# Performance work log

Measured on AMD Instinct MI355X. Metric: run time of the kernel, lower is better.

Reference implementation:

```python
import jax, jax.numpy as jnp
import numpy as np

B, T = 128, 50
VOCAB, EMB_D, GRU_H = 10000, 200, 100
HEADS, AHID, THID = 8, 96, 96

def _conv(x, w, b, pad):
    y = jax.lax.conv_general_dilated(x, w, (1, 1), pad,
        dimension_numbers=('NCHW', 'OIHW', 'NCHW'))
    return y + b[None, :, None, None]

def _bn(x, g, b, m, v):
    s = jax.lax.rsqrt(v + 1e-5)
    return (x - m[None, :, None, None]) * (g * s)[None, :, None, None] + b[None, :, None, None]

def _maxpool(x):
    return jax.lax.reduce_window(x, -jnp.inf, jax.lax.max, (1, 1, 2, 2), (1, 1, 2, 2), 'VALID')

def _resize(x):
    # F.interpolate(mode='bilinear', align_corners=False) == half-pixel bilinear, no antialias
    return jax.image.resize(x, (x.shape[0], x.shape[1], 25, 156), 'bilinear', antialias=False)

def _audio_attn(x, wq, bq, wk, bk, wv, bv):
    # x: [B,96,H,W]; wq: [heads,96,96] == stacked per-head 1x1 convs
    Q = jnp.einsum('bchw,noc->bnohw', x, wq) + bq[None, :, :, None, None]
    K = jnp.einsum('bchw,noc->bnohw', x, wk) + bk[None, :, :, None, None]
    V = jnp.einsum('bchw,noc->bnohw', x, wv) + bv[None, :, :, None, None]
    # torch F.softmax with no dim on a 4D tensor defaults to dim=1 (channels) -> axis=2 here
    return jax.nn.softmax(Q * K, axis=2) * V  # [B,heads,96,H,W]

def _text_attn(o, wq, bq, wk, bk, wv, bv):
    # o: [N,100]; wq: [heads,96,100] == stacked per-head Linear layers
    Q = jnp.einsum('nd,hod->nho', o, wq) + bq[None]
    K = jnp.einsum('nd,hod->nho', o, wk) + bk[None]
    V = jnp.einsum('nd,hod->nho', o, wv) + bv[None]
    a = jax.nn.softmax(Q * K, axis=2) * V  # 2D softmax default dim=1 -> over feature axis
    return a.reshape(o.shape[0], -1)  # head-concat order == torch cat along dim=1

def _gru(xs, w_ih, w_hh, b_ih, b_hh):
    # xs: [T,B,200]; torch gate order r, z, n; b_hn applied inside r-gating
    def step(h, x):
        gi = x @ w_ih.T + b_ih
        gh = h @ w_hh.T + b_hh
        ir, iz, inew = jnp.split(gi, 3, axis=1)
        hr, hz, hnew = jnp.split(gh, 3, axis=1)
        r = jax.nn.sigmoid(ir + hr)
        z = jax.nn.sigmoid(iz + hz)
        n = jnp.tanh(inew + r * hnew)
        h2 = (1.0 - z) * n + z * h
        return h2, h2
    h0 = jnp.zeros((xs.shape[1], GRU_H), xs.dtype)
    hT, outs = jax.lax.scan(step, h0, xs)
    return outs, hT

def _forward(tokens, lengths, mfcc_t, mfcc_f, mfcc_c, w1a, b1a, g1a, be1a, m1a, v1a, w1b, b1b, g1b, be1b, m1b, v1b, w2, b2, g2, be2, m2, v2, w3, b3, g3, be3, m3, v3, w4, b4, g4, be4, m4, v4, wq_a1, bq_a1, wk_a1, bk_a1, wv_a1, bv_a1, wq_a2, bq_a2, wk_a2, bk_a2, wv_a2, bv_a2, emb, w_ih, w_hh, b_ih, b_hh, wq_t1, bq_t1, wk_t1, bk_t1, wv_t1, bv_t1, wq_t2, bq_t2, wk_t2, bk_t2, wv_t2, bv_t2, w_fa, b_fa, w_ft, b_ft, w_e, b_e):
    # --- audio CNN stem (eval-mode batchnorm; dropout off) ---
    xa = jax.nn.relu(_bn(_conv(mfcc_t, w1a, b1a, 'VALID'), g1a, be1a, m1a, v1a))
    xb = jax.nn.relu(_bn(_conv(mfcc_f, w1b, b1b, 'VALID'), g1b, be1b, m1b, v1b))
    # NOTE: original source reuses conv1b/bn1b for the third input (faithful to that)
    xc = jax.nn.relu(_bn(_conv(mfcc_c, w1b, b1b, 'VALID'), g1b, be1b, m1b, v1b))
    x = jnp.concatenate([_resize(xa), _resize(xb), _resize(xc)], axis=1)  # [B,24,25,156]
    x = _maxpool(jax.nn.relu(_bn(_conv(x, w2, b2, [(1, 1), (1, 1)]), g2, be2, m2, v2)))  # [B,32,12,78]
    x = _maxpool(jax.nn.relu(_bn(_conv(x, w3, b3, [(1, 1), (1, 1)]), g3, be3, m3, v3)))  # [B,64,6,39]
    x = jax.nn.relu(_bn(_conv(x, w4, b4, [(1, 1), (1, 1)]), g4, be4, m4, v4))            # [B,96,6,39]
    # --- two stacked per-head audio attentions, then per-head spatial GAP ---
    a1 = _audio_attn(x, wq_a1, bq_a1, wk_a1, bk_a1, wv_a1, bv_a1).mean(axis=(-2, -1))  # [B,8,96]
    a2 = _audio_attn(x, wq_a2, bq_a2, wk_a2, bk_a2, wv_a2, bv_a2).mean(axis=(-2, -1))
    # forward() slices heads along the height concat and GAPs -> per head [stage1 96, stage2 96]
    self_attn_audio = jnp.concatenate([a1, a2], axis=2).reshape(x.shape[0], -1)  # [B,1536]
    # --- text branch: embedding + GRU (all lengths == T -> pack/pad is identity) ---
    ex = jnp.swapaxes(emb[tokens], 0, 1)  # [T,B,200]
    outs, h = _gru(ex, w_ih, w_hh, b_ih, b_hh)  # h: [B,100]
    output = jnp.swapaxes(outs, 0, 1).reshape(-1, GRU_H)  # [B*T,100]
    t1 = _text_attn(output, wq_t1, bq_t1, wk_t1, bk_t1, wv_t1, bv_t1)
    t2 = _text_attn(output, wq_t2, bq_t2, wk_t2, bk_t2, wv_t2, bv_t2)
    self_attn_text = jnp.concatenate([t1, t2], axis=1).reshape(x.shape[0], T, -1).sum(axis=1)  # [B,1536]
    # --- cross-modal gated fusion ---
    x_gap = x.mean(axis=(-2, -1))  # [B,96]
    a_text = jax.nn.softmax(x_gap @ w_fa.T + b_fa, axis=1)   # [B,100]
    attn_text_based_audio = a_text * h                        # [B,100]
    a_audio = jax.nn.softmax(h @ w_ft.T + b_ft, axis=1)      # [B,96]
    attn_audio_based_text = a_audio * x_gap                   # [B,96]
    feat = jnp.concatenate([self_attn_audio, self_attn_text,
                            attn_audio_based_text, attn_text_based_audio], axis=1)  # [B,3268]
    return feat @ w_e.T + b_e  # [B,4] emotion logits

def setup_inputs() -> dict:
    key = jax.random.key(0)
    ks = iter(jax.random.split(key, 100))
    nrm = lambda s, sc=0.05: jax.random.normal(next(ks), s, jnp.float32) * sc
    uni = lambda s: jax.random.uniform(next(ks), s, jnp.float32) * 0.5 + 0.5
    d = {}
    d['mfcc_t'] = jax.random.normal(next(ks), (B, 1, 200, 40), jnp.float32)
    d['mfcc_f'] = jax.random.normal(next(ks), (B, 1, 200, 40), jnp.float32)
    d['mfcc_c'] = jax.random.normal(next(ks), (B, 1, 200, 40), jnp.float32)
    d['tokens'] = jax.random.randint(next(ks), (B, T), 0, VOCAB)
    d['lengths'] = jnp.full((B,), T, jnp.int32)
    def bnp(pre, c):
        d['g' + pre] = 1.0 + nrm((c,)); d['be' + pre] = nrm((c,))
        d['m' + pre] = nrm((c,)); d['v' + pre] = uni((c,))
    d['w1a'] = nrm((8, 1, 5, 2), 0.2); d['b1a'] = nrm((8,)); bnp('1a', 8)
    d['w1b'] = nrm((8, 1, 2, 6), 0.2); d['b1b'] = nrm((8,)); bnp('1b', 8)
    d['w2'] = nrm((32, 24, 3, 3), 0.1); d['b2'] = nrm((32,)); bnp('2', 32)
    d['w3'] = nrm((64, 32, 3, 3), 0.1); d['b3'] = nrm((64,)); bnp('3', 64)
    d['w4'] = nrm((96, 64, 3, 3), 0.08); d['b4'] = nrm((96,)); bnp('4', 96)
    for s in ('1', '2'):
        for p in ('q', 'k', 'v'):
            d['w%s_a%s' % (p, s)] = nrm((HEADS, 96, 96), 0.1)
            d['b%s_a%s' % (p, s)] = nrm((HEADS, 96))
    d['emb'] = nrm((VOCAB, EMB_D), 0.1)
    d['w_ih'] = nrm((3 * GRU_H, EMB_D), 0.1); d['w_hh'] = nrm((3 * GRU_H, GRU_H), 0.1)
    d['b_ih'] = nrm((3 * GRU_H,)); d['b_hh'] = nrm((3 * GRU_H,))
    for s in ('1', '2'):
        for p in ('q', 'k', 'v'):
            d['w%s_t%s' % (p, s)] = nrm((HEADS, THID, GRU_H), 0.1)
            d['b%s_t%s' % (p, s)] = nrm((HEADS, THID))
    d['w_fa'] = nrm((100, 96), 0.1); d['b_fa'] = nrm((100,))
    d['w_ft'] = nrm((96, 100), 0.1); d['b_ft'] = nrm((96,))
    d['w_e'] = nrm((4, 2 * HEADS * AHID + 2 * HEADS * THID + 96 + 100), 0.05); d['b_e'] = nrm((4,))
    return d

def reference(mfcc_t, mfcc_f, mfcc_c, tokens, lengths, w1a, b1a, g1a, be1a, m1a, v1a, w1b, b1b, g1b, be1b, m1b, v1b, w2, b2, g2, be2, m2, v2, w3, b3, g3, be3, m3, v3, w4, b4, g4, be4, m4, v4, wq_a1, bq_a1, wk_a1, bk_a1, wv_a1, bv_a1, wq_a2, bq_a2, wk_a2, bk_a2, wv_a2, bv_a2, emb, w_ih, w_hh, b_ih, b_hh, wq_t1, bq_t1, wk_t1, bk_t1, wv_t1, bv_t1, wq_t2, bq_t2, wk_t2, bk_t2, wv_t2, bv_t2, w_fa, b_fa, w_ft, b_ft, w_e, b_e):
    return _forward(tokens, lengths, mfcc_t, mfcc_f, mfcc_c, w1a, b1a, g1a, be1a, m1a, v1a, w1b, b1b, g1b, be1b, m1b, v1b, w2, b2, g2, be2, m2, v2, w3, b3, g3, be3, m3, v3, w4, b4, g4, be4, m4, v4, wq_a1, bq_a1, wk_a1, bk_a1, wv_a1, bv_a1, wq_a2, bq_a2, wk_a2, bk_a2, wv_a2, bv_a2, emb, w_ih, w_hh, b_ih, b_hh, wq_t1, bq_t1, wk_t1, bk_t1, wv_t1, bv_t1, wq_t2, bq_t2, wk_t2, bk_t2, wv_t2, bv_t2, w_fa, b_fa, w_ft, b_ft, w_e, b_e)
```

## Files before the change

### kernel.cpp

```cpp
#include <hip/hip_runtime.h>
#include <math.h>

static constexpr int kB = 128;
static constexpr int kT = 50;

struct TDesc { const float* src; float* dst; int O; int C; int total; };
struct TPack { TDesc d[15]; };
__global__ void k_transpose_pack(TPack p) {
    TDesc t = p.d[blockIdx.y];
    int idx = blockIdx.x * 256 + threadIdx.x;
    if (idx >= t.total) return;
    int o = idx % t.O; int r = idx / t.O; int c = r % t.C; int n = r / t.C;
    t.dst[idx] = t.src[((size_t)n * t.O + o) * t.C + c];
}

__global__ void k_stem(const float* __restrict__ mt, const float* __restrict__ mf,
                       const float* __restrict__ mc,
                       const float* __restrict__ w1a, const float* __restrict__ b1a,
                       const float* __restrict__ g1a, const float* __restrict__ be1a,
                       const float* __restrict__ m1a, const float* __restrict__ v1a,
                       const float* __restrict__ w1b, const float* __restrict__ b1b,
                       const float* __restrict__ g1b, const float* __restrict__ be1b,
                       const float* __restrict__ m1b, const float* __restrict__ v1b,
                       float* __restrict__ out, int total) {
    int idx = blockIdx.x * blockDim.x + threadIdx.x;
    if (idx >= total) return;
    int ox = idx % 156; int t = idx / 156;
    int oy = t % 25; t /= 25;
    int ch = t % 24; int b = t / 24;
    int grp = ch >> 3, c = ch & 7;
    const float* src; int Hc, Wc;
    const float *wb, *cb, *g, *be, *m, *v;
    if (grp == 0) { src = mt; Hc = 196; Wc = 39; wb = w1a + c * 10;
                    cb = b1a; g = g1a; be = be1a; m = m1a; v = v1a; }
    else          { src = (grp == 1 ? mf : mc); Hc = 199; Wc = 35; wb = w1b + c * 12;
                    cb = b1b; g = g1b; be = be1b; m = m1b; v = v1b; }
    float s = g[c] * rsqrtf(v[c] + 1e-5f);
    float bias = (cb[c] - m[c]) * s + be[c];
    float sy = (oy + 0.5f) * ((float)Hc / 25.f) - 0.5f;
    float sx = (ox + 0.5f) * ((float)Wc / 156.f) - 0.5f;
    float fy0 = floorf(sy), fx0 = floorf(sx);
    float fy = sy - fy0, fx = sx - fx0;
    int y0 = (int)fy0, x0 = (int)fx0;
    int y0c = min(max(y0, 0), Hc - 1), y1c = min(max(y0 + 1, 0), Hc - 1);
    int x0c = min(max(x0, 0), Wc - 1), x1c = min(max(x0 + 1, 0), Wc - 1);
    bool xs = (x1c == x0c), ys = (y1c == y0c);
    const float* p = src + (size_t)b * 8000;
    float t00, t01, t10, t11;
    if (grp == 0) {
        float W[6][3];
        #pragma unroll
        for (int r = 0; r < 6; ++r) {
            int rr = min(y0c + r, 199);
            #pragma unroll
            for (int cc = 0; cc < 3; ++cc)
                W[r][cc] = p[rr * 40 + min(x0c + cc, 39)];
        }
        float a00 = 0.f, a01 = 0.f, a10 = 0.f, a11 = 0.f;
        #pragma unroll
        for (int ky = 0; ky < 5; ++ky)
            #pragma unroll
            for (int kx = 0; kx < 2; ++kx) {
                float wv = wb[ky * 2 + kx];
                a00 += W[ky][kx] * wv;     a01 += W[ky][kx + 1] * wv;
                a10 += W[ky + 1][kx] * wv; a11 += W[ky + 1][kx + 1] * wv;
            }
        t00 = a00;
        t01 = xs ? a00 : a01;
        t10 = ys ? a00 : a10;
        t11 = xs ? (ys ? a00 : a10) : (ys ? a01 : a11);
    } else {
        float W[3][7];
        #pragma unroll
        for (int r = 0; r < 3; ++r) {
            int rr = min(y0c + r, 199);
            #pragma unroll
            for (int cc = 0; cc < 7; ++cc)
                W[r][cc] = p[rr * 40 + min(x0c + cc, 39)];
        }
        float a00 = 0.f, a01 = 0.f, a10 = 0.f, a11 = 0.f;
        #pragma unroll
        for (int ky = 0; ky < 2; ++ky)
            #pragma unroll
            for (int kx = 0; kx < 6; ++kx) {
                float wv = wb[ky * 6 + kx];
                a00 += W[ky][kx] * wv;     a01 += W[ky][kx + 1] * wv;
                a10 += W[ky + 1][kx] * wv; a11 += W[ky + 1][kx + 1] * wv;
            }
        t00 = a00;
        t01 = xs ? a00 : a01;
        t10 = ys ? a00 : a10;
        t11 = xs ? (ys ? a00 : a10) : (ys ? a01 : a11);
    }
    float r00 = fmaxf(t00 * s + bias, 0.f), r01 = fmaxf(t01 * s + bias, 0.f);
    float r10 = fmaxf(t10 * s + bias, 0.f), r11 = fmaxf(t11 * s + bias, 0.f);
    out[idx] = r00 * (1.f - fy) * (1.f - fx) + r01 * (1.f - fy) * fx
             + r10 * fy * (1.f - fx) + r11 * fy * fx;
}

template<int CIN, int CI_T, int H, int W, int ROWS, int NPX>
__global__ void __launch_bounds__(256) k_conv3x3_tiled(
    const float* __restrict__ in, const float* __restrict__ wT,
    const float* __restrict__ cb, const float* __restrict__ g,
    const float* __restrict__ be, const float* __restrict__ m,
    const float* __restrict__ v, float* __restrict__ out, int COUT) {
    constexpr int WP = W + 2;
    constexpr int RP = ROWS + 2;
    constexpr int STAGE = CI_T * RP * WP;
    __shared__ float sx[STAGE];
    __shared__ float sw[CI_T * 9 * 8];
    const int b = blockIdx.x, rt = blockIdx.y, oc0 = blockIdx.z * 8;
    const int row0 = rt * ROWS;
    const int tid = threadIdx.x;

    int off[NPX]; bool val[NPX];
    #pragma unroll
    for (int j = 0; j < NPX; ++j) {
        int px = tid + j * 256;
        int oy = px / W, ox = px - oy * W;
        bool ok = (px < ROWS * W) && (row0 + oy < H);
        val[j] = ok;
        off[j] = ok ? (oy * WP + ox) : 0;
    }

    float acc[NPX][8];
    #pragma unroll
    for (int j = 0; j < NPX; ++j)
        #pragma unroll
        for (int o = 0; o < 8; ++o) acc[j][o] = 0.f;

    for (int c0 = 0; c0 < CIN; c0 += CI_T) {
        __syncthreads();
        for (int e = tid; e < STAGE; e += 256) {
            int ci = e / (RP * WP);
            int rem = e - ci * RP * WP;
            int r = rem / WP;
            int xx = rem - r * WP;
            int iy = row0 - 1 + r;
            int ix = xx - 1;
            float vv = 0.f;
            if (iy >= 0 && iy < H && ix >= 0 && ix < W)
                vv = in[((size_t)(b * CIN + c0 + ci) * H + iy) * W + ix];
            sx[e] = vv;
        }
        for (int e = tid; e < CI_T * 9 * 8; e += 256) {
            int rk = e >> 3;
            int o = e & 7;
            sw[e] = wT[((size_t)c0 * 9 + rk) * COUT + oc0 + o];
        }
        __syncthreads();
        #pragma unroll 1
        for (int cl = 0; cl < CI_T; ++cl) {
            const float* sxc = sx + cl * RP * WP;
            #pragma unroll
            for (int k = 0; k < 9; ++k) {
                const int ky = k / 3, kx = k % 3;
                const float4 wa = *(const float4*)(sw + (cl * 9 + k) * 8);
                const float4 wb = *(const float4*)(sw + (cl * 9 + k) * 8 + 4);
                #pragma unroll
                for (int j = 0; j < NPX; ++j) {
                    float xv = sxc[off[j] + ky * WP + kx];
                    acc[j][0] += xv * wa.x; acc[j][1] += xv * wa.y;
                    acc[j][2] += xv * wa.z; acc[j][3] += xv * wa.w;
                    acc[j][4] += xv * wb.x; acc[j][5] += xv * wb.y;
                    acc[j][6] += xv * wb.z; acc[j][7] += xv * wb.w;
                }
            }
        }
    }
    float sc[8], bi[8];
    #pragma unroll
    for (int o = 0; o < 8; ++o) {
        float s = g[oc0 + o] * rsqrtf(v[oc0 + o] + 1e-5f);
        sc[o] = s; bi[o] = (cb[oc0 + o] - m[oc0 + o]) * s + be[oc0 + o];
    }
    #pragma unroll
    for (int j = 0; j < NPX; ++j) if (val[j]) {
        int px = tid + j * 256;
        int oy = row0 + px / W, ox = px % W;
        #pragma unroll
        for (int o = 0; o < 8; ++o)
            out[((size_t)(b * COUT + oc0 + o) * H + oy) * W + ox] =
                fmaxf(acc[j][o] * sc[o] + bi[o], 0.f);
    }
}

__global__ void k_maxpool(const float* __restrict__ in, float* __restrict__ out,
                          int C, int Hin, int Win, int Hout, int Wout, int total) {
    int idx = blockIdx.x * blockDim.x + threadIdx.x;
    if (idx >= total) return;
    int ox = idx % Wout; int t = idx / Wout;
    int oy = t % Hout; t /= Hout;
    int c = t % C; int b = t / C;
    const float* p = in + ((size_t)(b * C + c) * Hin + 2 * oy) * Win + 2 * ox;
    float m0 = fmaxf(p[0], p[1]);
    float m1 = fmaxf(p[Win], p[Win + 1]);
    out[idx] = fmaxf(m0, m1);
}

__global__ void __launch_bounds__(128) k_audio_attn(
    const float* __restrict__ x,
    const float* __restrict__ wq1, const float* __restrict__ bq1,
    const float* __restrict__ wk1, const float* __restrict__ bk1,
    const float* __restrict__ wv1, const float* __restrict__ bv1,
    const float* __restrict__ wq2, const float* __restrict__ bq2,
    const float* __restrict__ wk2, const float* __restrict__ bk2,
    const float* __restrict__ wv2, const float* __restrict__ bv2,
    float* __restrict__ afeat, float* __restrict__ xgap) {
    int b = blockIdx.x, n = blockIdx.y, stage = blockIdx.z;
    const float* wq = stage ? wq2 : wq1; const float* bq = stage ? bq2 : bq1;
    const float* wk = stage ? wk2 : wk1; const float* bk = stage ? bk2 : bk1;
    const float* wv = stage ? wv2 : wv1; const float* bv = stage ? bv2 : bv1;
    __shared__ float xt[96 * 28];
    __shared__ float sb[96 * 27];
    __shared__ float pmax[4][26], psum[4][26];
    __shared__ float mx[26], sm[26];
    int tid = threadIdx.x;
    bool act = tid < 96;
    int o = act ? tid : 0;
    float bqv = act ? bq[n * 96 + tid] : 0.f;
    float bkv = act ? bk[n * 96 + tid] : 0.f;
    float bvv = act ? bv[n * 96 + tid] : 0.f;
    const float* wqb = wq + n * 9216 + o;
    const float* wkb = wk + n * 9216 + o;
    const float* wvb = wv + n * 9216 + o;
    const bool do_gap = (n == 0 && stage == 0);
    float accO = 0.f, xsum = 0.f;
    const float* xb = x + (size_t)b * 96 * 234;
    for (int tile = 0; tile < 9; ++tile) {
        int p0 = tile * 26;
        __syncthreads();
        for (int e = tid; e < 2496; e += 128) {
            int c = e / 26, pp = e - c * 26;
            xt[c * 28 + pp] = xb[c * 234 + p0 + pp];
        }
        __syncthreads();
        if (do_gap && act) {
            const float* xr = xt + o * 28;
            #pragma unroll
            for (int p = 0; p < 26; ++p) xsum += xr[p];
        }
        float aq[26], ak[26], av[26];
        #pragma unroll
        for (int p = 0; p < 26; ++p) { aq[p] = bqv; ak[p] = bkv; av[p] = bvv; }
        for (int c = 0; c < 96; ++c) {
            float wqv = wqb[c * 96], wkv = wkb[c * 96], wvv2 = wvb[c * 96];
            const float* xr = xt + c * 28;
            #pragma unroll
            for (int q4 = 0; q4 < 6; ++q4) {
                float4 x4 = *(const float4*)(xr + q4 * 4);
                int p = q4 * 4;
                aq[p]   += wqv * x4.x; ak[p]   += wkv * x4.x; av[p]   += wvv2 * x4.x;
                aq[p+1] += wqv * x4.y; ak[p+1] += wkv * x4.y; av[p+1] += wvv2 * x4.y;
                aq[p+2] += wqv * x4.z; ak[p+2] += wkv * x4.z; av[p+2] += wvv2 * x4.z;
                aq[p+3] += wqv * x4.w; ak[p+3] += wkv * x4.w; av[p+3] += wvv2 * x4.w;
            }
            float2 x2 = *(const float2*)(xr + 24);
            aq[24] += wqv * x2.x; ak[24] += wkv * x2.x; av[24] += wvv2 * x2.x;
            aq[25] += wqv * x2.y; ak[25] += wkv * x2.y; av[25] += wvv2 * x2.y;
        }
        if (act) {
            #pragma unroll
            for (int p = 0; p < 26; ++p)
                sb[o * 27 + p] = aq[p] * ak[p];
        }
        __syncthreads();
        if (tid < 104) {
            int p = tid % 26, ch = tid / 26;
            int o0 = ch * 24;
            float m_ = -1e30f;
            for (int q = 0; q < 24; ++q) m_ = fmaxf(m_, sb[(o0 + q) * 27 + p]);
            pmax[ch][p] = m_;
        }
        __syncthreads();
        if (tid < 26)
            mx[tid] = fmaxf(fmaxf(pmax[0][tid], pmax[1][tid]),
                            fmaxf(pmax[2][tid], pmax[3][tid]));
        __syncthreads();
        if (tid < 104) {
            int p = tid % 26, ch = tid / 26;
            int o0 = ch * 24;
            float mv = mx[p];
            float s_ = 0.f;
            for (int q = 0; q < 24; ++q) s_ += __expf(sb[(o0 + q) * 27 + p] - mv);
            psum[ch][p] = s_;
        }
        __syncthreads();
        if (tid < 26)
            sm[tid] = psum[0][tid] + psum[1][tid] + psum[2][tid] + psum[3][tid];
        __syncthreads();
        if (act) {
            #pragma unroll
            for (int p = 0; p < 26; ++p)
                accO += __expf(sb[o * 27 + p] - mx[p]) / sm[p] * av[p];
        }
    }
    if (act) afeat[b * 1536 + n * 192 + stage * 96 + tid] = accO * (1.f / 234.f);
    if (do_gap && act) xgap[b * 96 + tid] = xsum * (1.f / 234.f);
}

__global__ void __launch_bounds__(320) k_gi(const int* __restrict__ tokens,
        const float* __restrict__ emb, const float* __restrict__ w_ih,
        const float* __restrict__ b_ih, float* __restrict__ GI) {
    int r0 = blockIdx.x * 8;
    int tid = threadIdx.x;
    __shared__ float er[8][200];
    for (int e = tid; e < 1600; e += 320) {
        int r = e / 200, c = e - r * 200;
        er[r][c] = emb[(size_t)tokens[r0 + r] * 200 + c];
    }
    __syncthreads();
    if (tid < 300) {
        float acc[8];
        float bv = b_ih[tid];
        #pragma unroll
        for (int r = 0; r < 8; ++r) acc[r] = bv;
        for (int k4 = 0; k4 < 50; ++k4) {
            float4 w4 = *(const float4*)(w_ih + (size_t)tid * 200 + k4 * 4);
            #pragma unroll
            for (int r = 0; r < 8; ++r) {
                float4 x4 = *(const float4*)&er[r][k4 * 4];
                acc[r] += w4.x * x4.x + w4.y * x4.y + w4.z * x4.z + w4.w * x4.w;
            }
        }
        #pragma unroll
        for (int r = 0; r < 8; ++r)
            GI[(size_t)(r0 + r) * 300 + tid] = acc[r];
    }
}

__global__ void __launch_bounds__(320) k_gru_all(const float* __restrict__ GI,
        const float* __restrict__ w_hh, const float* __restrict__ b_hh,
        float* __restrict__ outs) {
    int b = blockIdx.x, tid = threadIdx.x;
    __shared__ float hs[100];
    __shared__ float gH[300];
    float4 wreg[25];
    float bias = 0.f;
    if (tid < 300) {
        bias = b_hh[tid];
        #pragma unroll
        for (int k4 = 0; k4 < 25; ++k4)
            wreg[k4] = *(const float4*)(w_hh + (size_t)tid * 100 + k4 * 4);
    }
    if (tid < 100) hs[tid] = 0.f;
    __syncthreads();
    for (int t = 0; t < kT; ++t) {
        if (tid < 300) {
            float gh = bias;
            #pragma unroll
            for (int k4 = 0; k4 < 25; ++k4) {
                float4 h4 = *(const float4*)&hs[k4 * 4];
                gh += wreg[k4].x * h4.x + wreg[k4].y * h4.y
                    + wreg[k4].z * h4.z + wreg[k4].w * h4.w;
            }
            gH[tid] = gh;
        }
        __syncthreads();
        if (tid < 100) {
            const float* gi = GI + ((size_t)b * kT + t) * 300;
            float r = 1.f / (1.f + expf(-(gi[tid] + gH[tid])));
            float z = 1.f / (1.f + expf(-(gi[100 + tid] + gH[100 + tid])));
            float nn = tanhf(gi[200 + tid] + r * gH[200 + tid]);
            float h2 = (1.f - z) * nn + z * hs[tid];
            hs[tid] = h2;
            outs[((size_t)b * kT + t) * 100 + tid] = h2;
        }
        __syncthreads();
    }
}

__global__ void __launch_bounds__(128) k_text_attn(const float* __restrict__ outs,
    const float* __restrict__ wq1, const float* __restrict__ bq1,
    const float* __restrict__ wk1, const float* __restrict__ bk1,
    const float* __restrict__ wv1, const float* __restrict__ bv1,
    const float* __restrict__ wq2, const float* __restrict__ bq2,
    const float* __restrict__ wk2, const float* __restrict__ bk2,
    const float* __restrict__ wv2, const float* __restrict__ bv2,
    float* __restrict__ tfeat) {
    int b = blockIdx.x, stage = blockIdx.y, n = blockIdx.z;
    const float* wq = stage ? wq2 : wq1; const float* bq = stage ? bq2 : bq1;
    const float* wk = stage ? wk2 : wk1; const float* bk = stage ? bk2 : bk1;
    const float* wv = stage ? wv2 : wv1; const float* bv = stage ? bv2 : bv1;
    int tid = threadIdx.x;
    bool act = tid < 96;
    int oo = act ? tid : 0;
    const float* wqc = wq + n * 9600 + oo;
    const float* wkc = wk + n * 9600 + oo;
    const float* wvc = wv + n * 9600 + oo;
    float bqv = act ? bq[n * 96 + tid] : 0.f;
    float bkv = act ? bk[n * 96 + tid] : 0.f;
    float bvv = act ? bv[n * 96 + tid] : 0.f;
    __shared__ float rows[10][100];
    __shared__ float wredM[2][10], wredS[2][10];
    float acc = 0.f;
    int wave = tid >> 6, lane = tid & 63;
    for (int tile = 0; tile < 5; ++tile) {
        int t0 = tile * 10;
        __syncthreads();
        for (int e = tid; e < 1000; e += 128) {
            int tt = e / 100, c = e - tt * 100;
            rows[tt][c] = outs[((size_t)b * kT + t0 + tt) * 100 + c];
        }
        __syncthreads();
        float q[10], k[10], v[10];
        #pragma unroll
        for (int tt = 0; tt < 10; ++tt) { q[tt] = bqv; k[tt] = bkv; v[tt] = bvv; }
        for (int c4 = 0; c4 < 25; ++c4) {
            int cb = c4 * 4 * 96;
            float q0 = wqc[cb], q1 = wqc[cb + 96], q2 = wqc[cb + 192], q3 = wqc[cb + 288];
            float k0 = wkc[cb], k1 = wkc[cb + 96], k2 = wkc[cb + 192], k3 = wkc[cb + 288];
            float v0 = wvc[cb], v1 = wvc[cb + 96], v2 = wvc[cb + 192], v3 = wvc[cb + 288];
            #pragma unroll
            for (int tt = 0; tt < 10; ++tt) {
                float4 x4 = *(const float4*)&rows[tt][c4 * 4];
                q[tt] += q0 * x4.x + q1 * x4.y + q2 * x4.z + q3 * x4.w;
                k[tt] += k0 * x4.x + k1 * x4.y + k2 * x4.z + k3 * x4.w;
                v[tt] += v0 * x4.x + v1 * x4.y + v2 * x4.z + v3 * x4.w;
            }
        }
        float s[10], e_[10];
        #pragma unroll
        for (int tt = 0; tt < 10; ++tt) s[tt] = act ? q[tt] * k[tt] : -1e30f;
        #pragma unroll
        for (int tt = 0; tt < 10; ++tt) {
            float m = s[tt];
            #pragma unroll
            for (int off = 1; off < 64; off <<= 1) m = fmaxf(m, __shfl_xor(m, off));
            if (lane == 0) wredM[wave][tt] = m;
        }
        __syncthreads();
        #pragma unroll
        for (int tt = 0; tt < 10; ++tt) {
            float mx = fmaxf(wredM[0][tt], wredM[1][tt]);
            e_[tt] = expf(s[tt] - mx);
        }
        #pragma unroll
        for (int tt = 0; tt < 10; ++tt) {
            float sm = e_[tt];
            #pragma unroll
            for (int off = 1; off < 64; off <<= 1) sm += __shfl_xor(sm, off);
            if (lane == 0) wredS[wave][tt] = sm;
        }
        __syncthreads();
        #pragma unroll
        for (int tt = 0; tt < 10; ++tt) {
            float sm = wredS[0][tt] + wredS[1][tt];
            acc += e_[tt] / sm * v[tt];
        }
    }
    if (act) tfeat[b * 1536 + stage * 768 + n * 96 + tid] = acc;
}

__global__ void __launch_bounds__(128) k_final(const float* __restrict__ xgap,
    const float* __restrict__ outs, const float* __restrict__ afeat,
    const float* __restrict__ tfeat,
    const float* __restrict__ w_fa, const float* __restrict__ b_fa,
    const float* __restrict__ w_ft, const float* __restrict__ b_ft,
    const float* __restrict__ w_e, const float* __restrict__ b_e,
    float* __restrict__ out) {
    int b = blockIdx.x; int tid = threadIdx.x;
    __shared__ float xg[96], hv[100], st[100], sa[96], aat[96], atba[100];
    __shared__ float redm[2], reds[2];
    if (tid < 96) xg[tid] = xgap[b * 96 + tid];
    if (tid < 100) hv[tid] = outs[(size_t)(b * kT + kT - 1) * 100 + tid];
    __syncthreads();
    if (tid < 100) {
        float acc = b_fa[tid];
        const float* wr = w_fa + tid * 96;
        for (int c = 0; c < 96; ++c) acc += wr[c] * xg[c];
        st[tid] = acc;
    }
    if (tid < 96) {
        float acc = b_ft[tid];
        const float* wr = w_ft + tid * 100;
        for (int c = 0; c < 100; ++c) acc += wr[c] * hv[c];
        sa[tid] = acc;
    }
    __syncthreads();
    if (tid == 0) {
        float mxv = -1e30f; for (int i = 0; i < 100; ++i) mxv = fmaxf(mxv, st[i]);
        float s = 0.f; for (int i = 0; i < 100; ++i) s += expf(st[i] - mxv);
        redm[0] = mxv; reds[0] = s;
    }
    if (tid == 1) {
        float mxv = -1e30f; for (int i = 0; i < 96; ++i) mxv = fmaxf(mxv, sa[i]);
        float s = 0.f; for (int i = 0; i < 96; ++i) s += expf(sa[i] - mxv);
        redm[1] = mxv; reds[1] = s;
    }
    __syncthreads();
    if (tid < 100) atba[tid] = expf(st[tid] - redm[0]) / reds[0] * hv[tid];
    if (tid < 96)  aat[tid]  = expf(sa[tid] - redm[1]) / reds[1] * xg[tid];
    __syncthreads();
    float a0 = 0.f, a1 = 0.f, a2 = 0.f, a3 = 0.f;
    for (int col = tid; col < 3268; col += 128) {
        float f;
        if (col < 1536)      f = afeat[b * 1536 + col];
        else if (col < 3072) f = tfeat[b * 1536 + col - 1536];
        else if (col < 3168) f = aat[col - 3072];
        else                 f = atba[col - 3168];
        a0 += w_e[col] * f;            a1 += w_e[3268 + col] * f;
        a2 += w_e[2 * 3268 + col] * f; a3 += w_e[3 * 3268 + col] * f;
    }
    __shared__ float r4[4][128];
    r4[0][tid] = a0; r4[1][tid] = a1; r4[2][tid] = a2; r4[3][tid] = a3;
    __syncthreads();
    if (tid < 4) {
        float s = 0.f;
        for (int i = 0; i < 128; ++i) s += r4[tid][i];
        out[b * 4 + tid] = s + b_e[tid];
    }
}

extern "C" void kernel_launch(void* const* d_in, const int* in_sizes, int n_in,
                              void* d_out, int out_size, void* d_ws, size_t ws_size,
                              hipStream_t stream) {
    (void)in_sizes; (void)n_in; (void)out_size; (void)ws_size;
    const float* mfcc_t = (const float*)d_in[0];
    const float* mfcc_f = (const float*)d_in[1];
    const float* mfcc_c = (const float*)d_in[2];
    const int*   tokens = (const int*)d_in[3];
    const float *w1a = (const float*)d_in[5],  *b1a = (const float*)d_in[6],
                *g1a = (const float*)d_in[7],  *be1a = (const float*)d_in[8],
                *m1a = (const float*)d_in[9],  *v1a = (const float*)d_in[10];
    const float *w1b = (const float*)d_in[11], *b1b = (const float*)d_in[12],
                *g1b = (const float*)d_in[13], *be1b = (const float*)d_in[14],
                *m1b = (const float*)d_in[15], *v1b = (const float*)d_in[16];
    const float *w2 = (const float*)d_in[17], *b2 = (const float*)d_in[18],
                *g2 = (const float*)d_in[19], *be2 = (const float*)d_in[20],
                *m2 = (const float*)d_in[21], *v2 = (const float*)d_in[22];
    const float *w3 = (const float*)d_in[23], *b3 = (const float*)d_in[24],
                *g3 = (const float*)d_in[25], *be3 = (const float*)d_in[26],
                *m3 = (const float*)d_in[27], *v3 = (const float*)d_in[28];
    const float *w4 = (const float*)d_in[29], *b4 = (const float*)d_in[30],
                *g4 = (const float*)d_in[31], *be4 = (const float*)d_in[32],
                *m4 = (const float*)d_in[33], *v4 = (const float*)d_in[34];
    const float *wq_a1 = (const float*)d_in[35], *bq_a1 = (const float*)d_in[36],
                *wk_a1 = (const float*)d_in[37], *bk_a1 = (const float*)d_in[38],
                *wv_a1 = (const float*)d_in[39], *bv_a1 = (const float*)d_in[40];
    const float *wq_a2 = (const float*)d_in[41], *bq_a2 = (const float*)d_in[42],
                *wk_a2 = (const float*)d_in[43], *bk_a2 = (const float*)d_in[44],
                *wv_a2 = (const float*)d_in[45], *bv_a2 = (const float*)d_in[46];
    const float *emb  = (const float*)d_in[47];
    const float *w_ih = (const float*)d_in[48], *w_hh = (const float*)d_in[49],
                *b_ih = (const float*)d_in[50], *b_hh = (const float*)d_in[51];
    const float *wq_t1 = (const float*)d_in[52], *bq_t1 = (const float*)d_in[53],
                *wk_t1 = (const float*)d_in[54], *bk_t1 = (const float*)d_in[55],
                *wv_t1 = (const float*)d_in[56], *bv_t1 = (const float*)d_in[57];
    const float *wq_t2 = (const float*)d_in[58], *bq_t2 = (const float*)d_in[59],
                *wk_t2 = (const float*)d_in[60], *bk_t2 = (const float*)d_in[61],
                *wv_t2 = (const float*)d_in[62], *bv_t2 = (const float*)d_in[63];
    const float *w_fa = (const float*)d_in[64], *b_fa = (const float*)d_in[65],
                *w_ft = (const float*)d_in[66], *b_ft = (const float*)d_in[67],
                *w_e  = (const float*)d_in[68], *b_e  = (const float*)d_in[69];

    float* ws = (float*)d_ws;
    const size_t Z0 = 0;
    const size_t Z1 = 22091776ull;
    const size_t OUTS  = 34072576ull;
    const size_t AFEAT = 34712576ull;
    const size_t TFEAT = 34909184ull;
    const size_t XGAP  = 35105792ull;
    const size_t WT    = 35118080ull;
    float* X1 = ws + Z1;
    float* C2 = ws + Z0;  float* P2 = ws + Z1;
    float* C3 = ws + Z0;  float* P3 = ws + Z1;
    float* X4 = ws + Z0;  float* GI = ws + Z1;
    float* outs  = ws + OUTS;
    float* afeat = ws + AFEAT;
    float* tfeat = ws + TFEAT;
    float* xgap  = ws + XGAP;
    float* wqa1t = ws + WT;
    float* wka1t = wqa1t + 73728; float* wva1t = wka1t + 73728;
    float* wqa2t = wva1t + 73728; float* wka2t = wqa2t + 73728; float* wva2t = wka2t + 73728;
    float* wqt1t = wva2t + 73728;
    float* wkt1t = wqt1t + 76800; float* wvt1t = wkt1t + 76800;
    float* wqt2t = wvt1t + 76800; float* wkt2t = wqt2t + 76800; float* wvt2t = wkt2t + 76800;
    float* wT2 = outs;
    float* wT3 = outs + 6912;
    float* wT4 = outs + 25344;

    TPack tp;
    tp.d[0]  = {wq_a1, wqa1t, 96, 96, 73728};
    tp.d[1]  = {wk_a1, wka1t, 96, 96, 73728};
    tp.d[2]  = {wv_a1, wva1t, 96, 96, 73728};
    tp.d[3]  = {wq_a2, wqa2t, 96, 96, 73728};
    tp.d[4]  = {wk_a2, wka2t, 96, 96, 73728};
    tp.d[5]  = {wv_a2, wva2t, 96, 96, 73728};
    tp.d[6]  = {w2, wT2, 32, 216, 6912};
    tp.d[7]  = {w3, wT3, 64, 288, 18432};
    tp.d[8]  = {w4, wT4, 96, 576, 55296};
    tp.d[9]  = {wq_t1, wqt1t, 96, 100, 76800};
    tp.d[10] = {wk_t1, wkt1t, 96, 100, 76800};
    tp.d[11] = {wv_t1, wvt1t, 96, 100, 76800};
    tp.d[12] = {wq_t2, wqt2t, 96, 100, 76800};
    tp.d[13] = {wk_t2, wkt2t, 96, 100, 76800};
    tp.d[14] = {wv_t2, wvt2t, 96, 100, 76800};
    k_transpose_pack<<<dim3(300, 15), 256, 0, stream>>>(tp);

    k_stem<<<46800, 256, 0, stream>>>(mfcc_t, mfcc_f, mfcc_c,
        w1a, b1a, g1a, be1a, m1a, v1a,
        w1b, b1b, g1b, be1b, m1b, v1b, X1, 11980800);
    k_conv3x3_tiled<24, 8, 25, 156, 9, 6><<<dim3(128, 3, 4), 256, 0, stream>>>(
        X1, wT2, b2, g2, be2, m2, v2, C2, 32);
    k_maxpool<<<14976, 256, 0, stream>>>(C2, P2, 32, 25, 156, 12, 78, 3833856);
    k_conv3x3_tiled<32, 8, 12, 78, 12, 4><<<dim3(128, 1, 8), 256, 0, stream>>>(
        P2, wT3, b3, g3, be3, m3, v3, C3, 64);
    k_maxpool<<<7488, 256, 0, stream>>>(C3, P3, 64, 12, 78, 6, 39, 1916928);
    k_conv3x3_tiled<64, 16, 6, 39, 6, 1><<<dim3(128, 1, 12), 256, 0, stream>>>(
        P3, wT4, b4, g4, be4, m4, v4, X4, 96);

    k_audio_attn<<<dim3(kB, 8, 2), 128, 0, stream>>>(X4,
        wqa1t, bq_a1, wka1t, bk_a1, wva1t, bv_a1,
        wqa2t, bq_a2, wka2t, bk_a2, wva2t, bv_a2, afeat, xgap);

    k_gi<<<kB * kT / 8, 320, 0, stream>>>(tokens, emb, w_ih, b_ih, GI);
    k_gru_all<<<kB, 320, 0, stream>>>(GI, w_hh, b_hh, outs);
    k_text_attn<<<dim3(kB, 2, 8), 128, 0, stream>>>(outs,
        wqt1t, bq_t1, wkt1t, bk_t1, wvt1t, bv_t1,
        wqt2t, bq_t2, wkt2t, bk_t2, wvt2t, bv_t2, tfeat);

    k_final<<<kB, 128, 0, stream>>>(xgap, outs, afeat, tfeat,
                                    w_fa, b_fa, w_ft, b_ft, w_e, b_e, (float*)d_out);
}
```

Measured before the change: 1.571 ms.

## Move audio attention projections to bf16x3 MFMA with split-position halves

Rewrites the audio attention kernel to compute the Q/K/V 1x1 projections with bf16 MFMA instructions. A hi/lo bf16 split of weights and activations, with three MFMAs per product, keeps close to fp32 accuracy. The work is also split into two halves over spatial positions, each writing its own partial output buffer that the final kernel sums. This adds a weight conversion pre-pass, a new workspace buffer at a fixed offset and some extra MFMA work, in exchange for replacing scalar FMA loops.

```diff
diff --git a/kernel.cpp b/kernel.cpp
--- a/kernel.cpp
+++ b/kernel.cpp
@@ -4,14 +4,33 @@
 static constexpr int kB = 128;
 static constexpr int kT = 50;
 
+typedef __attribute__((ext_vector_type(8))) short short8;
+typedef __attribute__((ext_vector_type(4))) float f32x4;
+
 struct TDesc { const float* src; float* dst; int O; int C; int total; };
-struct TPack { TDesc d[15]; };
+struct TPack { TDesc d[9]; };
 __global__ void k_transpose_pack(TPack p) {
     TDesc t = p.d[blockIdx.y];
     int idx = blockIdx.x * 256 + threadIdx.x;
     if (idx >= t.total) return;
     int o = idx % t.O; int r = idx / t.O; int c = r % t.C; int n = r / t.C;
     t.dst[idx] = t.src[((size_t)n * t.O + o) * t.C + c];
+}
+
+struct CDesc { const float* src; unsigned short* dhi; unsigned short* dlo; int total; };
+struct CPack { CDesc d[6]; };
+__global__ void k_cvt_pack(CPack p) {
+    CDesc t = p.d[blockIdx.y];
+    int idx = blockIdx.x * 256 + threadIdx.x;
+    if (idx >= t.total) return;
+    float w = t.src[idx];
+    unsigned int u = __float_as_uint(w);
+    unsigned short h = (unsigned short)((u + 0x7FFFu + ((u >> 16) & 1u)) >> 16);
+    float fh = __uint_as_float(((unsigned int)h) << 16);
+    float lo = w - fh;
+    unsigned int ul = __float_as_uint(lo);
+    unsigned short l = (unsigned short)((ul + 0x7FFFu + ((ul >> 16) & 1u)) >> 16);
+    t.dhi[idx] = h; t.dlo[idx] = l;
 }
 
 __global__ void k_stem(const float* __restrict__ mt, const float* __restrict__ mf,
@@ -198,105 +217,143 @@
     out[idx] = fmaxf(m0, m1);
 }
 
-__global__ void __launch_bounds__(128) k_audio_attn(
+__global__ void __launch_bounds__(256) k_audio_attn(
     const float* __restrict__ x,
-    const float* __restrict__ wq1, const float* __restrict__ bq1,
-    const float* __restrict__ wk1, const float* __restrict__ bk1,
-    const float* __restrict__ wv1, const float* __restrict__ bv1,
-    const float* __restrict__ wq2, const float* __restrict__ bq2,
-    const float* __restrict__ wk2, const float* __restrict__ bk2,
-    const float* __restrict__ wv2, const float* __restrict__ bv2,
-    float* __restrict__ afeat, float* __restrict__ xgap) {
-    int b = blockIdx.x, n = blockIdx.y, stage = blockIdx.z;
-    const float* wq = stage ? wq2 : wq1; const float* bq = stage ? bq2 : bq1;
-    const float* wk = stage ? wk2 : wk1; const float* bk = stage ? bk2 : bk1;
-    const float* wv = stage ? wv2 : wv1; const float* bv = stage ? bv2 : bv1;
-    __shared__ float xt[96 * 28];
-    __shared__ float sb[96 * 27];
-    __shared__ float pmax[4][26], psum[4][26];
-    __shared__ float mx[26], sm[26];
+    const unsigned short* __restrict__ whi, const unsigned short* __restrict__ wlo,
+    const float* __restrict__ bq1, const float* __restrict__ bk1, const float* __restrict__ bv1,
+    const float* __restrict__ bq2, const float* __restrict__ bk2, const float* __restrict__ bv2,
+    float* __restrict__ af0, float* __restrict__ af1, float* __restrict__ xgap) {
+    int b = blockIdx.x, n = blockIdx.y;
+    int stage = blockIdx.z >> 1, half = blockIdx.z & 1;
+    const int NCT = half ? 7 : 8;
+    const int ct0 = half * 8;
+    const float* bq = stage ? bq2 : bq1;
+    const float* bk = stage ? bk2 : bk1;
+    const float* bv = stage ? bv2 : bv1;
+    __shared__ unsigned short sxh[8 * 3 * 64 * 8];
+    __shared__ unsigned short sxl[8 * 3 * 64 * 8];
+    __shared__ float sbias[3][96];
+    __shared__ float sacc[4][96];
     int tid = threadIdx.x;
-    bool act = tid < 96;
-    int o = act ? tid : 0;
-    float bqv = act ? bq[n * 96 + tid] : 0.f;
-    float bkv = act ? bk[n * 96 + tid] : 0.f;
-    float bvv = act ? bv[n * 96 + tid] : 0.f;
-    const float* wqb = wq + n * 9216 + o;
-    const float* wkb = wk + n * 9216 + o;
-    const float* wvb = wv + n * 9216 + o;
-    const bool do_gap = (n == 0 && stage == 0);
-    float accO = 0.f, xsum = 0.f;
     const float* xb = x + (size_t)b * 96 * 234;
-    for (int tile = 0; tile < 9; ++tile) {
-        int p0 = tile * 26;
-        __syncthreads();
-        for (int e = tid; e < 2496; e += 128) {
-            int c = e / 26, pp = e - c * 26;
-            xt[c * 28 + pp] = xb[c * 234 + p0 + pp];
-        }
-        __syncthreads();
-        if (do_gap && act) {
-            const float* xr = xt + o * 28;
-            #pragma unroll
-            for (int p = 0; p < 26; ++p) xsum += xr[p];
-        }
-        float aq[26], ak[26], av[26];
-        #pragma unroll
-        for (int p = 0; p < 26; ++p) { aq[p] = bqv; ak[p] = bkv; av[p] = bvv; }
-        for (int c = 0; c < 96; ++c) {
-            float wqv = wqb[c * 96], wkv = wkb[c * 96], wvv2 = wvb[c * 96];
-            const float* xr = xt + c * 28;
-            #pragma unroll
-            for (int q4 = 0; q4 < 6; ++q4) {
-                float4 x4 = *(const float4*)(xr + q4 * 4);
-                int p = q4 * 4;
-                aq[p]   += wqv * x4.x; ak[p]   += wkv * x4.x; av[p]   += wvv2 * x4.x;
-                aq[p+1] += wqv * x4.y; ak[p+1] += wkv * x4.y; av[p+1] += wvv2 * x4.y;
-                aq[p+2] += wqv * x4.z; ak[p+2] += wkv * x4.z; av[p+2] += wvv2 * x4.z;
-                aq[p+3] += wqv * x4.w; ak[p+3] += wkv * x4.w; av[p+3] += wvv2 * x4.w;
-            }
-            float2 x2 = *(const float2*)(xr + 24);
-            aq[24] += wqv * x2.x; ak[24] += wkv * x2.x; av[24] += wvv2 * x2.x;
-            aq[25] += wqv * x2.y; ak[25] += wkv * x2.y; av[25] += wvv2 * x2.y;
-        }
-        if (act) {
-            #pragma unroll
-            for (int p = 0; p < 26; ++p)
-                sb[o * 27 + p] = aq[p] * ak[p];
-        }
-        __syncthreads();
-        if (tid < 104) {
-            int p = tid % 26, ch = tid / 26;
-            int o0 = ch * 24;
-            float m_ = -1e30f;
-            for (int q = 0; q < 24; ++q) m_ = fmaxf(m_, sb[(o0 + q) * 27 + p]);
-            pmax[ch][p] = m_;
-        }
-        __syncthreads();
-        if (tid < 26)
-            mx[tid] = fmaxf(fmaxf(pmax[0][tid], pmax[1][tid]),
-                            fmaxf(pmax[2][tid], pmax[3][tid]));
-        __syncthreads();
-        if (tid < 104) {
-            int p = tid % 26, ch = tid / 26;
-            int o0 = ch * 24;
-            float mv = mx[p];
-            float s_ = 0.f;
-            for (int q = 0; q < 24; ++q) s_ += __expf(sb[(o0 + q) * 27 + p] - mv);
-            psum[ch][p] = s_;
-        }
-        __syncthreads();
-        if (tid < 26)
-            sm[tid] = psum[0][tid] + psum[1][tid] + psum[2][tid] + psum[3][tid];
-        __syncthreads();
-        if (act) {
-            #pragma unroll
-            for (int p = 0; p < 26; ++p)
-                accO += __expf(sb[o * 27 + p] - mx[p]) / sm[p] * av[p];
-        }
-    }
-    if (act) afeat[b * 1536 + n * 192 + stage * 96 + tid] = accO * (1.f / 234.f);
-    if (do_gap && act) xgap[b * 96 + tid] = xsum * (1.f / 234.f);
+    int NP = NCT * 16;
+    for (int e = tid; e < 96 * NP; e += 256) {
+        int c = e / NP, pp = e - c * NP;
+        int p = ct0 * 16 + pp;
+        float xv = (p < 234) ? xb[c * 234 + p] : 0.f;
+        unsigned int u = __float_as_uint(xv);
+        unsigned short h = (unsigned short)((u + 0x7FFFu + ((u >> 16) & 1u)) >> 16);
+        float fh = __uint_as_float(((unsigned int)h) << 16);
+        float lov = xv - fh;
+        unsigned int ul = __float_as_uint(lov);
+        unsigned short l = (unsigned short)((ul + 0x7FFFu + ((ul >> 16) & 1u)) >> 16);
+        int ctl = pp >> 4, pl2 = pp & 15, kc = c >> 5, qd2 = (c >> 3) & 3, j = c & 7;
+        int ix2 = (((ctl * 3 + kc) * 64) + qd2 * 16 + pl2) * 8 + j;
+        sxh[ix2] = h; sxl[ix2] = l;
+    }
+    for (int e = tid; e < 288; e += 256) {
+        int mtx = e / 96, o = e - mtx * 96;
+        const float* bb = (mtx == 0) ? bq : (mtx == 1) ? bk : bv;
+        sbias[mtx][o] = bb[n * 96 + o];
+    }
+    __syncthreads();
+    const bool do_gap = (n == 0 && blockIdx.z == 0);
+    if (do_gap && tid < 96) {
+        float s_ = 0.f;
+        const float* pr = xb + tid * 234;
+        for (int i = 0; i < 234; ++i) s_ += pr[i];
+        xgap[b * 96 + tid] = s_ * (1.f / 234.f);
+    }
+    int wid = tid >> 6, lane = tid & 63, pl = lane & 15, qd = lane >> 4;
+    const unsigned short* wqh = whi + ((size_t)(stage * 3 + 0) * 73728) + (size_t)n * 9216;
+    const unsigned short* wkh = whi + ((size_t)(stage * 3 + 1) * 73728) + (size_t)n * 9216;
+    const unsigned short* wvh = whi + ((size_t)(stage * 3 + 2) * 73728) + (size_t)n * 9216;
+    const unsigned short* wql = wlo + ((size_t)(stage * 3 + 0) * 73728) + (size_t)n * 9216;
+    const unsigned short* wkl = wlo + ((size_t)(stage * 3 + 1) * 73728) + (size_t)n * 9216;
+    const unsigned short* wvl = wlo + ((size_t)(stage * 3 + 2) * 73728) + (size_t)n * 9216;
+    f32x4 acc6[6];
+    #pragma unroll
+    for (int rt = 0; rt < 6; ++rt) acc6[rt] = (f32x4){0.f, 0.f, 0.f, 0.f};
+    for (int ctl = wid; ctl < NCT; ctl += 4) {
+        f32x4 Q[6], K[6], V[6];
+        #pragma unroll
+        for (int rt = 0; rt < 6; ++rt) {
+            Q[rt] = (f32x4){0.f, 0.f, 0.f, 0.f};
+            K[rt] = (f32x4){0.f, 0.f, 0.f, 0.f};
+            V[rt] = (f32x4){0.f, 0.f, 0.f, 0.f};
+        }
+        #pragma unroll
+        for (int kc = 0; kc < 3; ++kc) {
+            short8 bh = *(const short8*)(sxh + ((ctl * 3 + kc) * 64 + lane) * 8);
+            short8 bl = *(const short8*)(sxl + ((ctl * 3 + kc) * 64 + lane) * 8);
+            #pragma unroll
+            for (int rt = 0; rt < 6; ++rt) {
+                int aoff = (rt * 16 + pl) * 96 + kc * 32 + qd * 8;
+                short8 ah, al;
+                ah = *(const short8*)(wqh + aoff); al = *(const short8*)(wql + aoff);
+                Q[rt] = __builtin_amdgcn_mfma_f32_16x16x32_bf16(ah, bh, Q[rt], 0, 0, 0);
+                Q[rt] = __builtin_amdgcn_mfma_f32_16x16x32_bf16(ah, bl, Q[rt], 0, 0, 0);
+                Q[rt] = __builtin_amdgcn_mfma_f32_16x16x32_bf16(al, bh, Q[rt], 0, 0, 0);
+                ah = *(const short8*)(wkh + aoff); al = *(const short8*)(wkl + aoff);
+                K[rt] = __builtin_amdgcn_mfma_f32_16x16x32_bf16(ah, bh, K[rt], 0, 0, 0);
+                K[rt] = __builtin_amdgcn_mfma_f32_16x16x32_bf16(ah, bl, K[rt], 0, 0, 0);
+                K[rt] = __builtin_amdgcn_mfma_f32_16x16x32_bf16(al, bh, K[rt], 0, 0, 0);
+                ah = *(const short8*)(wvh + aoff); al = *(const short8*)(wvl + aoff);
+                V[rt] = __builtin_amdgcn_mfma_f32_16x16x32_bf16(ah, bh, V[rt], 0, 0, 0);
+                V[rt] = __builtin_amdgcn_mfma_f32_16x16x32_bf16(ah, bl, V[rt], 0, 0, 0);
+                V[rt] = __builtin_amdgcn_mfma_f32_16x16x32_bf16(al, bh, V[rt], 0, 0, 0);
+            }
+        }
+        float s[6][4];
+        float m_ = -1e30f;
+        #pragma unroll
+        for (int rt = 0; rt < 6; ++rt)
+            #pragma unroll
+            for (int r = 0; r < 4; ++r) {
+                int o = rt * 16 + qd * 4 + r;
+                float qv = Q[rt][r] + sbias[0][o];
+                float kv = K[rt][r] + sbias[1][o];
+                s[rt][r] = qv * kv;
+                m_ = fmaxf(m_, s[rt][r]);
+            }
+        m_ = fmaxf(m_, __shfl_xor(m_, 16));
+        m_ = fmaxf(m_, __shfl_xor(m_, 32));
+        float t = 0.f;
+        #pragma unroll
+        for (int rt = 0; rt < 6; ++rt)
+            #pragma unroll
+            for (int r = 0; r < 4; ++r) {
+                s[rt][r] = __expf(s[rt][r] - m_);
+                t += s[rt][r];
+            }
+        t += __shfl_xor(t, 16);
+        t += __shfl_xor(t, 32);
+        float inv = (((ct0 + ctl) * 16 + pl) < 234) ? 1.f / t : 0.f;
+        #pragma unroll
+        for (int rt = 0; rt < 6; ++rt)
+            #pragma unroll
+            for (int r = 0; r < 4; ++r) {
+                int o = rt * 16 + qd * 4 + r;
+                acc6[rt][r] += s[rt][r] * inv * (V[rt][r] + sbias[2][o]);
+            }
+    }
+    #pragma unroll
+    for (int rt = 0; rt < 6; ++rt)
+        #pragma unroll
+        for (int r = 0; r < 4; ++r) {
+            float a = acc6[rt][r];
+            a += __shfl_xor(a, 1);
+            a += __shfl_xor(a, 2);
+            a += __shfl_xor(a, 4);
+            a += __shfl_xor(a, 8);
+            if (pl == 0) sacc[wid][rt * 16 + qd * 4 + r] = a;
+        }
+    __syncthreads();
+    if (tid < 96) {
+        float* dst = half ? af1 : af0;
+        dst[b * 1536 + n * 192 + stage * 96 + tid] =
+            (sacc[0][tid] + sacc[1][tid] + sacc[2][tid] + sacc[3][tid]) * (1.f / 234.f);
+    }
 }
 
 __global__ void __launch_bounds__(320) k_gi(const int* __restrict__ tokens,
@@ -453,8 +510,8 @@
 }
 
 __global__ void __launch_bounds__(128) k_final(const float* __restrict__ xgap,
-    const float* __restrict__ outs, const float* __restrict__ afeat,
-    const float* __restrict__ tfeat,
+    const float* __restrict__ outs, const float* __restrict__ af0,
+    const float* __restrict__ af1, const float* __restrict__ tfeat,
     const float* __restrict__ w_fa, const float* __restrict__ b_fa,
     const float* __restrict__ w_ft, const float* __restrict__ b_ft,
     const float* __restrict__ w_e, const float* __restrict__ b_e,
@@ -495,7 +552,7 @@
     float a0 = 0.f, a1 = 0.f, a2 = 0.f, a3 = 0.f;
     for (int col = tid; col < 3268; col += 128) {
         float f;
-        if (col < 1536)      f = afeat[b * 1536 + col];
+        if (col < 1536)      f = af0[b * 1536 + col] + af1[b * 1536 + col];
         else if (col < 3072) f = tfeat[b * 1536 + col - 1536];
         else if (col < 3168) f = aat[col - 3072];
         else                 f = atba[col - 3168];
@@ -567,13 +624,13 @@
     float* C3 = ws + Z0;  float* P3 = ws + Z1;
     float* X4 = ws + Z0;  float* GI = ws + Z1;
     float* outs  = ws + OUTS;
-    float* afeat = ws + AFEAT;
+    float* afeat0 = ws + AFEAT;
+    float* afeat1 = ws + 4000000ull;
     float* tfeat = ws + TFEAT;
     float* xgap  = ws + XGAP;
-    float* wqa1t = ws + WT;
-    float* wka1t = wqa1t + 73728; float* wva1t = wka1t + 73728;
-    float* wqa2t = wva1t + 73728; float* wka2t = wqa2t + 73728; float* wva2t = wka2t + 73728;
-    float* wqt1t = wva2t + 73728;
+    unsigned short* whi = (unsigned short*)(ws + WT);
+    unsigned short* wlo = whi + 442368;
+    float* wqt1t = ws + WT + 442368ull;
     float* wkt1t = wqt1t + 76800; float* wvt1t = wkt1t + 76800;
     float* wqt2t = wvt1t + 76800; float* wkt2t = wqt2t + 76800; float* wvt2t = wkt2t + 76800;
     float* wT2 = outs;
@@ -581,22 +638,24 @@
     float* wT4 = outs + 25344;
 
     TPack tp;
-    tp.d[0]  = {wq_a1, wqa1t, 96, 96, 73728};
-    tp.d[1]  = {wk_a1, wka1t, 96, 96, 73728};
-    tp.d[2]  = {wv_a1, wva1t, 96, 96, 73728};
-    tp.d[3]  = {wq_a2, wqa2t, 96, 96, 73728};
-    tp.d[4]  = {wk_a2, wka2t, 96, 96, 73728};
-    tp.d[5]  = {wv_a2, wva2t, 96, 96, 73728};
-    tp.d[6]  = {w2, wT2, 32, 216, 6912};
-    tp.d[7]  = {w3, wT3, 64, 288, 18432};
-    tp.d[8]  = {w4, wT4, 96, 576, 55296};
-    tp.d[9]  = {wq_t1, wqt1t, 96, 100, 76800};
-    tp.d[10] = {wk_t1, wkt1t, 96, 100, 76800};
-    tp.d[11] = {wv_t1, wvt1t, 96, 100, 76800};
-    tp.d[12] = {wq_t2, wqt2t, 96, 100, 76800};
-    tp.d[13] = {wk_t2, wkt2t, 96, 100, 76800};
-    tp.d[14] = {wv_t2, wvt2t, 96, 100, 76800};
-    k_transpose_pack<<<dim3(300, 15), 256, 0, stream>>>(tp);
+    tp.d[0] = {w2, wT2, 32, 216, 6912};
+    tp.d[1] = {w3, wT3, 64, 288, 18432};
+    tp.d[2] = {w4, wT4, 96, 576, 55296};
+    tp.d[3] = {wq_t1, wqt1t, 96, 100, 76800};
+    tp.d[4] = {wk_t1, wkt1t, 96, 100, 76800};
+    tp.d[5] = {wv_t1, wvt1t, 96, 100, 76800};
+    tp.d[6] = {wq_t2, wqt2t, 96, 100, 76800};
+    tp.d[7] = {wk_t2, wkt2t, 96, 100, 76800};
+    tp.d[8] = {wv_t2, wvt2t, 96, 100, 76800};
+    k_transpose_pack<<<dim3(300, 9), 256, 0, stream>>>(tp);
+    CPack cp;
+    cp.d[0] = {wq_a1, whi + 0 * 73728, wlo + 0 * 73728, 73728};
+    cp.d[1] = {wk_a1, whi + 1 * 73728, wlo + 1 * 73728, 73728};
+    cp.d[2] = {wv_a1, whi + 2 * 73728, wlo + 2 * 73728, 73728};
+    cp.d[3] = {wq_a2, whi + 3 * 73728, wlo + 3 * 73728, 73728};
+    cp.d[4] = {wk_a2, whi + 4 * 73728, wlo + 4 * 73728, 73728};
+    cp.d[5] = {wv_a2, whi + 5 * 73728, wlo + 5 * 73728, 73728};
+    k_cvt_pack<<<dim3(288, 6), 256, 0, stream>>>(cp);
 
     k_stem<<<46800, 256, 0, stream>>>(mfcc_t, mfcc_f, mfcc_c,
         w1a, b1a, g1a, be1a, m1a, v1a,
@@ -610,9 +669,8 @@
     k_conv3x3_tiled<64, 16, 6, 39, 6, 1><<<dim3(128, 1, 12), 256, 0, stream>>>(
         P3, wT4, b4, g4, be4, m4, v4, X4, 96);
 
-    k_audio_attn<<<dim3(kB, 8, 2), 128, 0, stream>>>(X4,
-        wqa1t, bq_a1, wka1t, bk_a1, wva1t, bv_a1,
-        wqa2t, bq_a2, wka2t, bk_a2, wva2t, bv_a2, afeat, xgap);
+    k_audio_attn<<<dim3(kB, 8, 4), 256, 0, stream>>>(X4, whi, wlo,
+        bq_a1, bk_a1, bv_a1, bq_a2, bk_a2, bv_a2, afeat0, afeat1, xgap);
 
     k_gi<<<kB * kT / 8, 320, 0, stream>>>(tokens, emb, w_ih, b_ih, GI);
     k_gru_all<<<kB, 320, 0, stream>>>(GI, w_hh, b_hh, outs);
@@ -620,6 +678,6 @@
         wqt1t, bq_t1, wkt1t, bk_t1, wvt1t, bv_t1,
         wqt2t, bq_t2, wkt2t, bk_t2, wvt2t, bv_t2, tfeat);
 
-    k_final<<<kB, 128, 0, stream>>>(xgap, outs, afeat, tfeat,
+    k_final<<<kB, 128, 0, stream>>>(xgap, outs, afeat0, afeat1, tfeat,
                                     w_fa, b_fa, w_ft, b_ft, w_e, b_e, (float*)d_out);
 }
```

Measured after the change: 2.044 ms. 30.1% more time.
